# Performance work log

Hardware: AMD Instinct MI355X
Metric: run time of the kernel (lower is better)

Reference implementation:

```python
import jax, jax.numpy as jnp
import numpy as np

N_IMG, N_CAP, N_RGN, MAX_W, EMBED = 32, 32, 36, 50, 1024
LAMBDA_SOFTMAX = 9.0
NORM_EPS = 1e-12  # F.normalize default eps


def setup_inputs() -> dict:
    key = jax.random.key(0)
    ks = jax.random.split(key, 13)
    rgn = jax.random.normal(ks[0], (N_IMG, N_RGN, EMBED), jnp.float32)
    img = jax.random.normal(ks[1], (N_IMG, EMBED), jnp.float32)
    wrd = jax.random.normal(ks[2], (N_CAP, MAX_W, EMBED), jnp.float32)
    stc = jax.random.normal(ks[3], (N_CAP, EMBED), jnp.float32)
    # ragged caption lengths in [1, MAX_W]
    stc_lens = jax.random.randint(ks[4], (N_CAP,), 1, MAX_W + 1, dtype=jnp.int32)
    s = 1.0 / np.sqrt(EMBED)
    w_scale = jax.random.normal(ks[5], (EMBED, EMBED), jnp.float32) * s
    b_scale = jnp.zeros((EMBED,), jnp.float32)
    w_shift = jax.random.normal(ks[6], (EMBED, EMBED), jnp.float32) * s
    b_shift = jnp.zeros((EMBED,), jnp.float32)
    w1 = jax.random.normal(ks[7], (EMBED, EMBED), jnp.float32) * s
    b1 = jnp.zeros((EMBED,), jnp.float32)
    w2 = jax.random.normal(ks[8], (EMBED, EMBED), jnp.float32) * s
    b2 = jnp.zeros((EMBED,), jnp.float32)
    return dict(rgn=rgn, img=img, wrd=wrd, stc=stc, stc_lens=stc_lens,
                w_scale=w_scale, b_scale=b_scale, w_shift=w_shift, b_shift=b_shift,
                w1=w1, b1=b1, w2=w2, b2=b2)


def reference(rgn, img, wrd, stc, stc_lens, w_scale, b_scale, w_shift, b_shift, w1, b1, w2, b2):
    # rgn: (I, Q, D) regions; wrd: (C, L, D) ragged words; stc_lens: (C,)
    C, L, D = wrd.shape
    valid = jnp.arange(L)[None, :] < stc_lens[:, None]          # (C, L)
    # scores[c,i,l,q] = wrd[c,l] . rgn[i,q]  (bmm(context, queryT))
    s = jnp.einsum('cld,iqd->cilq', wrd, rgn)                   # (C, I, L, Q)
    s = jnp.where(s >= 0, s, 0.1 * s)                           # LeakyReLU(0.1)
    # L2-normalize over the query (region) axis, per (c,i,l)
    s = s / jnp.maximum(jnp.sqrt(jnp.sum(s * s, axis=3, keepdims=True)), NORM_EPS)
    # temperature softmax over valid words (ragged mask)
    logits = jnp.where(valid[:, None, :, None], s * LAMBDA_SOFTMAX, -jnp.inf)
    attn = jax.nn.softmax(logits, axis=2)                       # (C, I, L, Q)
    # weightedContext[c,i,q,d] = sum_l attn * wrd
    wei = jnp.einsum('cilq,cld->ciqd', attn, wrd)               # (C, I, Q, D)
    # FiLM-style refine
    scaling = jnp.tanh(jnp.einsum('ciqd,ed->ciqe', wei, w_scale) + b_scale)
    shifting = jnp.einsum('ciqd,ed->ciqe', wei, w_shift) + b_shift
    x = rgn[None] * scaling + shifting                          # (C, I, Q, D)
    h = jax.nn.relu(jnp.einsum('ciqd,ed->ciqe', x, w1) + b1)
    modu = jnp.einsum('ciqd,ed->ciqe', h, w2) + b2
    ref = modu + rgn[None]
    # torch cats per-caption results along dim=1 -> (I, C, Q, D)
    return jnp.transpose(ref, (1, 0, 2, 3))
```

## Files before the change

kernel.cpp:

```cpp
#include <hip/hip_runtime.h>
#include <math.h>

#define NC 32
#define NI 32
#define NL 50
#define NQ 36
#define ND 1024
#define LAMBDA 9.0f

#define BM 128
#define BN 128

typedef __attribute__((ext_vector_type(8))) short bf16x8;
typedef __attribute__((ext_vector_type(4))) float floatx4;

static __device__ __forceinline__ unsigned short f2b(float f) {
    unsigned int u = __float_as_uint(f);
    unsigned int r = (u + 0x7fffu + ((u >> 16) & 1u)) >> 16;
    return (unsigned short)r;
}
static __device__ __forceinline__ float bf2f(unsigned short u) {
    return __uint_as_float(((unsigned int)u) << 16);
}

static __device__ __forceinline__ float ftanh(float x) {
    float ax = fabsf(x);
    float e = __expf(ax + ax);
    return copysignf(1.f - 2.f / (e + 1.f), x);
}

static __device__ __forceinline__ void gload16(const unsigned short* g, unsigned short* l) {
    __builtin_amdgcn_global_load_lds(
        (const __attribute__((address_space(1))) unsigned int*)g,
        (__attribute__((address_space(3))) unsigned int*)l, 16, 0, 0);
}

struct CvtJob { const float* src; unsigned short* dst; int n2; int valid2; };
struct CvtJobs { CvtJob j[4]; };

__global__ __launch_bounds__(256) void k_cvt(CvtJobs jobs) {
    CvtJob jb = jobs.j[blockIdx.y];
    unsigned int* d32 = (unsigned int*)jb.dst;
    int stride = gridDim.x * 256;
    for (int i = blockIdx.x * 256 + threadIdx.x; i < jb.n2; i += stride) {
        unsigned int pk = 0;
        if (i < jb.valid2) {
            float2 v = ((const float2*)jb.src)[i];
            pk = (unsigned int)f2b(v.x) | ((unsigned int)f2b(v.y) << 16);
        }
        d32[i] = pk;
    }
}

struct HlJob { const float* src; unsigned short* hi; unsigned short* lo; int n2; };
struct HlJobs { HlJob j[2]; };

__global__ __launch_bounds__(256) void k_cvt_hilo(HlJobs jobs) {
    HlJob jb = jobs.j[blockIdx.y];
    unsigned int* h32 = (unsigned int*)jb.hi;
    unsigned int* l32 = (unsigned int*)jb.lo;
    int stride = gridDim.x * 256;
    for (int i = blockIdx.x * 256 + threadIdx.x; i < jb.n2; i += stride) {
        float2 v = ((const float2*)jb.src)[i];
        unsigned short h0 = f2b(v.x), h1 = f2b(v.y);
        unsigned short l0 = f2b(v.x - bf2f(h0)), l1 = f2b(v.y - bf2f(h1));
        h32[i] = (unsigned int)h0 | ((unsigned int)h1 << 16);
        l32[i] = (unsigned int)l0 | ((unsigned int)l1 << 16);
    }
}

#define SST 37

__global__ __launch_bounds__(256) void k_attn(
    const unsigned short* __restrict__ whi, const unsigned short* __restrict__ wlo,
    const unsigned short* __restrict__ rhi, const unsigned short* __restrict__ rlo,
    const int* __restrict__ lens, unsigned short* __restrict__ attn)
{
    int bx = blockIdx.x;
    int c = bx / NI, i = bx % NI;
    __shared__ __align__(16) unsigned short Wh[64 * 32], Wl[64 * 32];
    __shared__ __align__(16) unsigned short Rh[48 * 32], Rl[48 * 32];
    __shared__ float S[64 * SST];
    int t = threadIdx.x, lane = t & 63, wid = t >> 6;
    int lrow = lane & 15, quad = lane >> 4;
    int len = lens[c];

    int grow = lane >> 2;
    int ssw = ((lane & 3) ^ ((lane >> 3) & 3)) * 8;
    const unsigned short* garr = (wid == 0) ? whi : (wid == 1) ? wlo : (wid == 2) ? rhi : rlo;
    unsigned short* larr = (wid == 0) ? Wh : (wid == 1) ? Wl : (wid == 2) ? Rh : Rl;
    int ngroups = (wid < 2) ? 4 : 3;
    size_t gbase = (wid < 2) ? (size_t)(c * NL) * ND : (size_t)(i * NQ) * ND;

    floatx4 acc[3] = {};
    int fsw = (quad ^ ((lrow >> 1) & 3)) * 8;

    for (int kt = 0; kt < ND; kt += 32) {
        for (int j = 0; j < ngroups; ++j) {
            int row = j * 16 + grow;
            gload16(garr + gbase + (size_t)row * ND + kt + ssw, larr + j * 512 + lane * 8);
        }
        __syncthreads();
        bf16x8 ah = *(const bf16x8*)&Wh[(wid * 16 + lrow) * 32 + fsw];
        bf16x8 al = *(const bf16x8*)&Wl[(wid * 16 + lrow) * 32 + fsw];
#pragma unroll
        for (int nt = 0; nt < 3; ++nt) {
            bf16x8 bh = *(const bf16x8*)&Rh[(nt * 16 + lrow) * 32 + fsw];
            bf16x8 bl = *(const bf16x8*)&Rl[(nt * 16 + lrow) * 32 + fsw];
            acc[nt] = __builtin_amdgcn_mfma_f32_16x16x32_bf16(ah, bh, acc[nt], 0, 0, 0);
            acc[nt] = __builtin_amdgcn_mfma_f32_16x16x32_bf16(ah, bl, acc[nt], 0, 0, 0);
            acc[nt] = __builtin_amdgcn_mfma_f32_16x16x32_bf16(al, bh, acc[nt], 0, 0, 0);
        }
        __syncthreads();
    }
#pragma unroll
    for (int nt = 0; nt < 3; ++nt) {
        int q = nt * 16 + lrow;
        if (q < NQ) {
#pragma unroll
            for (int r = 0; r < 4; ++r) {
                int l = wid * 16 + quad * 4 + r;
                S[l * SST + q] = acc[nt][r];
            }
        }
    }
    __syncthreads();
    if (t < 200) {
        int l = t >> 2, part = t & 3;
        float lv[9];
        float ss = 0.f;
#pragma unroll
        for (int jj = 0; jj < 9; ++jj) {
            int q = part * 9 + jj;
            float v = S[l * SST + q];
            float x = (v >= 0.f) ? v : 0.1f * v;
            lv[jj] = x;
            ss += x * x;
        }
        ss += __shfl_xor(ss, 1);
        ss += __shfl_xor(ss, 2);
        float inv = LAMBDA / fmaxf(sqrtf(ss), 1e-12f);
#pragma unroll
        for (int jj = 0; jj < 9; ++jj) S[l * SST + part * 9 + jj] = lv[jj] * inv;
    }
    __syncthreads();
    if (t < 144) {
        int q = t >> 2, part = t & 3;
        int ls = part * 13;
        int le = ls + 13 < len ? ls + 13 : len;
        float m = -1e30f;
        for (int l = ls; l < le; ++l) m = fmaxf(m, S[l * SST + q]);
        m = fmaxf(m, __shfl_xor(m, 1));
        m = fmaxf(m, __shfl_xor(m, 2));
        float sum = 0.f;
        for (int l = ls; l < le; ++l) sum += __expf(S[l * SST + q] - m);
        sum += __shfl_xor(sum, 1);
        sum += __shfl_xor(sum, 2);
        float inv = 1.f / sum;
        unsigned int* o = (unsigned int*)attn + ((size_t)(c * NI + i) * NQ + q) * 32;
        int jb = part * 8;
#pragma unroll
        for (int jj = 0; jj < 8; ++jj) {
            int j = jb + jj;
            int l0 = 2 * j, l1 = 2 * j + 1;
            unsigned short a0 = (l0 < len) ? f2b(__expf(S[l0 * SST + q] - m) * inv) : (unsigned short)0;
            unsigned short a1 = (l1 < len) ? f2b(__expf(S[l1 * SST + q] - m) * inv) : (unsigned short)0;
            o[j] = (unsigned int)a0 | ((unsigned int)a1 << 16);
        }
    }
}

__global__ __launch_bounds__(256, 2) void k_pgemm(
    const unsigned short* __restrict__ A, const unsigned short* __restrict__ B1,
    const unsigned short* __restrict__ B2, unsigned short* __restrict__ P1,
    unsigned short* __restrict__ P2)
{
    const int K = ND;
    const int BK = 32;
    int bn = blockIdx.x, bm = blockIdx.y;
    const unsigned short* B = blockIdx.z ? B2 : B1;
    unsigned short* P = blockIdx.z ? P2 : P1;
    int m0 = bm * BM, n0 = bn * BN;

    __shared__ __align__(16) unsigned short At[BM * 32];
    __shared__ __align__(16) unsigned short Bt[BN * 32];

    int t = threadIdx.x, lane = t & 63, wid = t >> 6;
    int wx = wid & 1, wy = wid >> 1;
    int lrow = lane & 15, quad = lane >> 4;
    floatx4 acc[4][4] = {};

    int srow = t >> 2, pos = t & 3;
    int ssw = (pos ^ ((srow >> 1) & 3)) * 8;
    const unsigned short* Aptr = A + (size_t)(m0 + srow) * K + ssw;
    const unsigned short* Bptr = B + (size_t)(n0 + srow) * K + ssw;
    unsigned short* Al  = &At[srow * BK + pos * 8];
    unsigned short* Al2 = &At[(srow + 64) * BK + pos * 8];
    unsigned short* Bl  = &Bt[srow * BK + pos * 8];
    unsigned short* Bl2 = &Bt[(srow + 64) * BK + pos * 8];
    int fsw = (quad ^ ((lrow >> 1) & 3)) * 8;

    for (int kt = 0; kt < K; kt += BK) {
        gload16(Aptr + kt, Al);
        gload16(Aptr + (size_t)64 * K + kt, Al2);
        gload16(Bptr + kt, Bl);
        gload16(Bptr + (size_t)64 * K + kt, Bl2);
        __syncthreads();
        bf16x8 af[4], bfr[4];
#pragma unroll
        for (int im = 0; im < 4; ++im)
            af[im] = *(const bf16x8*)&At[(wy * 64 + im * 16 + lrow) * BK + fsw];
#pragma unroll
        for (int in = 0; in < 4; ++in)
            bfr[in] = *(const bf16x8*)&Bt[(wx * 64 + in * 16 + lrow) * BK + fsw];
#pragma unroll
        for (int im = 0; im < 4; ++im)
#pragma unroll
            for (int in = 0; in < 4; ++in)
                acc[im][in] = __builtin_amdgcn_mfma_f32_16x16x32_bf16(
                    af[im], bfr[in], acc[im][in], 0, 0, 0);
        __syncthreads();
    }
#pragma unroll
    for (int im = 0; im < 4; ++im)
#pragma unroll
        for (int in = 0; in < 4; ++in) {
            int n = n0 + wx * 64 + in * 16 + lrow;
#pragma unroll
            for (int r = 0; r < 4; ++r) {
                int m = m0 + wy * 64 + im * 16 + quad * 4 + r;
                int c = m / NL, l = m - c * NL;
                if (c < NC) P[((size_t)(c * ND + n)) * 64 + l] = f2b(acc[im][in][r]);
            }
        }
}

__global__ __launch_bounds__(256, 2) void k_attn_gemm(
    const unsigned short* __restrict__ attn, const unsigned short* __restrict__ Psc,
    const unsigned short* __restrict__ Psh, const float* __restrict__ bsc,
    const float* __restrict__ bsh, const float* __restrict__ rgnf,
    unsigned short* __restrict__ xbuf)
{
    int bn = blockIdx.x, bm = blockIdx.y, c = blockIdx.z;
    __shared__ __align__(16) unsigned short smem3[3 * 128 * 64];
    unsigned short* At  = smem3;
    unsigned short* B1t = smem3 + 8192;
    unsigned short* B2t = smem3 + 16384;
    unsigned short* Ct  = smem3;
    int t = threadIdx.x, lane = t & 63, wid = t >> 6;
    int wx = wid & 1, wy = wid >> 1;
    int lrow = lane & 15, quad = lane >> 4;
    int grow = lane >> 3, pos = lane & 7;

    const unsigned short* Ab  = attn + (size_t)(c * 1152 + bm * 128) * 64;
    const unsigned short* B1b = Psc + (size_t)(c * ND + bn * 128) * 64;
    const unsigned short* B2b = Psh + (size_t)(c * ND + bn * 128) * 64;
    for (int g = wid; g < 16; g += 4) {
        int row = g * 8 + grow;
        int ssw = (pos ^ (row & 7)) * 8;
        gload16(Ab + (size_t)row * 64 + ssw, &At[g * 512 + lane * 8]);
        gload16(B1b + (size_t)row * 64 + ssw, &B1t[g * 512 + lane * 8]);
        gload16(B2b + (size_t)row * 64 + ssw, &B2t[g * 512 + lane * 8]);
    }
    __syncthreads();

    floatx4 acc[4][4] = {}, acc2[4][4] = {};
#pragma unroll
    for (int kk = 0; kk < 2; ++kk) {
        int sw = ((kk * 4 + quad) ^ (lrow & 7)) * 8;
        bf16x8 af[4], b1f[4], b2f[4];
#pragma unroll
        for (int im = 0; im < 4; ++im)
            af[im] = *(const bf16x8*)&At[(wy * 64 + im * 16 + lrow) * 64 + sw];
#pragma unroll
        for (int in = 0; in < 4; ++in) {
            b1f[in] = *(const bf16x8*)&B1t[(wx * 64 + in * 16 + lrow) * 64 + sw];
            b2f[in] = *(const bf16x8*)&B2t[(wx * 64 + in * 16 + lrow) * 64 + sw];
        }
#pragma unroll
        for (int im = 0; im < 4; ++im)
#pragma unroll
            for (int in = 0; in < 4; ++in) {
                acc[im][in] = __builtin_amdgcn_mfma_f32_16x16x32_bf16(
                    af[im], b1f[in], acc[im][in], 0, 0, 0);
                acc2[im][in] = __builtin_amdgcn_mfma_f32_16x16x32_bf16(
                    af[im], b2f[in], acc2[im][in], 0, 0, 0);
            }
    }
    __syncthreads();
#pragma unroll
    for (int im = 0; im < 4; ++im)
#pragma unroll
        for (int in = 0; in < 4; ++in) {
            int n = bn * 128 + wx * 64 + in * 16 + lrow;
            float b1v = bsc[n], b2v = bsh[n];
#pragma unroll
            for (int r = 0; r < 4; ++r) {
                int row = wy * 64 + im * 16 + quad * 4 + r;
                int m = bm * 128 + row;
                int i = m / NQ, q = m - i * NQ;
                float sc = ftanh(acc[im][in][r] + b1v);
                float sh = acc2[im][in][r] + b2v;
                float rg = rgnf[(size_t)(i * NQ + q) * ND + n];
                int colc = (wx * 8 + in * 2 + (lrow >> 3)) ^ (row & 7);
                Ct[row * 128 + colc * 8 + (lrow & 7)] = f2b(rg * sc + sh);
            }
        }
    __syncthreads();
#pragma unroll
    for (int p = 0; p < 8; ++p) {
        int row = p * 16 + (t >> 4), chunk = t & 15;
        int m = bm * 128 + row;
        int i = m / NQ, q = m - i * NQ;
        size_t dr = ((size_t)(i * NC + c) * NQ + q) * ND + bn * 128 + chunk * 8;
        *(bf16x8*)&xbuf[dr] = *(const bf16x8*)&Ct[row * 128 + ((chunk ^ (row & 7)) * 8)];
    }
}

template <int MODE, int MINW>
__global__ __launch_bounds__(256, MINW) void k_gemm(
    const unsigned short* __restrict__ A, const unsigned short* __restrict__ B1,
    const float* __restrict__ bias1, const float* __restrict__ rgnf,
    void* __restrict__ outp)
{
    const int K = ND;
    int lin = blockIdx.x;
    int xcd = lin & 7;
    int kb = lin >> 3;
    int bm = xcd * 36 + (kb >> 3);
    int bn = kb & 7;
    int m0 = bm * BM, n0 = bn * BN;

    __shared__ __align__(16) unsigned short smem[2 * 128 * 64];
    unsigned short* At = smem;
    unsigned short* Bt = smem + 8192;
    unsigned short* Ct = smem;

    int t = threadIdx.x;
    int lane = t & 63, wid = t >> 6;
    int wx = wid & 1, wy = wid >> 1;
    int lrow = lane & 15, quad = lane >> 4;

    floatx4 acc[4][4] = {};

    int srow = t >> 3, pos = t & 7;
    int ssw = (pos ^ (srow & 7)) * 8;
    const unsigned short* Aptr  = A  + (size_t)(m0 + srow) * K + ssw;
    const unsigned short* B1ptr = B1 + (size_t)(n0 + srow) * K + ssw;
    unsigned short* ldA = At + t * 8;
    unsigned short* ldB = Bt + t * 8;

    for (int kt = 0; kt < K; kt += 64) {
#pragma unroll
        for (int p = 0; p < 4; ++p) {
            gload16(Aptr + (size_t)(p * 32) * K + kt, ldA + p * 2048);
            gload16(B1ptr + (size_t)(p * 32) * K + kt, ldB + p * 2048);
        }
        __syncthreads();
#pragma unroll
        for (int kh = 0; kh < 2; ++kh) {
            int sw = ((kh * 4 + quad) ^ (lrow & 7)) * 8;
            bf16x8 af[4], bfr[4];
#pragma unroll
            for (int im = 0; im < 4; ++im)
                af[im] = *(const bf16x8*)&At[(wy * 64 + im * 16 + lrow) * 64 + sw];
#pragma unroll
            for (int in = 0; in < 4; ++in)
                bfr[in] = *(const bf16x8*)&Bt[(wx * 64 + in * 16 + lrow) * 64 + sw];
#pragma unroll
            for (int im = 0; im < 4; ++im)
#pragma unroll
                for (int in = 0; in < 4; ++in)
                    acc[im][in] = __builtin_amdgcn_mfma_f32_16x16x32_bf16(
                        af[im], bfr[in], acc[im][in], 0, 0, 0);
        }
        __syncthreads();
    }

    if constexpr (MODE == 1) {
#pragma unroll
        for (int im = 0; im < 4; ++im)
#pragma unroll
            for (int in = 0; in < 4; ++in) {
                int n = n0 + wx * 64 + in * 16 + lrow;
                float b1v = bias1[n];
#pragma unroll
                for (int r = 0; r < 4; ++r) {
                    int row = wy * 64 + im * 16 + quad * 4 + r;
                    float h = acc[im][in][r] + b1v;
                    h = h > 0.f ? h : 0.f;
                    int colc = (wx * 8 + in * 2 + (lrow >> 3)) ^ (row & 7);
                    Ct[row * 128 + colc * 8 + (lrow & 7)] = f2b(h);
                }
            }
        __syncthreads();
        unsigned short* ob = (unsigned short*)outp + (size_t)m0 * ND + n0;
#pragma unroll
        for (int p = 0; p < 8; ++p) {
            int row = p * 16 + (t >> 4), chunk = t & 15;
            *(bf16x8*)&ob[(size_t)row * ND + chunk * 8] =
                *(const bf16x8*)&Ct[row * 128 + ((chunk ^ (row & 7)) * 8)];
        }
    } else {
#pragma unroll
        for (int im = 0; im < 4; ++im)
#pragma unroll
            for (int in = 0; in < 4; ++in) {
                int n = n0 + wx * 64 + in * 16 + lrow;
                float b1v = bias1[n];
#pragma unroll
                for (int r = 0; r < 4; ++r) {
                    int m = m0 + wy * 64 + im * 16 + quad * 4 + r;
                    int i = m / (NC * NQ);
                    int q = m % NQ;
                    float rg = rgnf[(size_t)(i * NQ + q) * ND + n];
                    ((float*)outp)[(size_t)m * ND + n] = acc[im][in][r] + b1v + rg;
                }
            }
    }
}

extern "C" void kernel_launch(void* const* d_in, const int* in_sizes, int n_in,
                              void* d_out, int out_size, void* d_ws, size_t ws_size,
                              hipStream_t stream) {
    const float* rgn     = (const float*)d_in[0];
    const float* wrd     = (const float*)d_in[2];
    const int*   lens    = (const int*)d_in[4];
    const float* w_scale = (const float*)d_in[5];
    const float* b_scale = (const float*)d_in[6];
    const float* w_shift = (const float*)d_in[7];
    const float* b_shift = (const float*)d_in[8];
    const float* w1      = (const float*)d_in[9];
    const float* b1      = (const float*)d_in[10];
    const float* w2      = (const float*)d_in[11];
    const float* b2      = (const float*)d_in[12];
    float* outf = (float*)d_out;

    char* ws = (char*)d_ws;
    unsigned short* wsc_bf = (unsigned short*)(ws + 0);
    unsigned short* wsh_bf = (unsigned short*)(ws + 2097152);
    unsigned short* w1_bf  = (unsigned short*)(ws + 4194304);
    unsigned short* w2_bf  = (unsigned short*)(ws + 6291456);
    unsigned short* attn   = (unsigned short*)(ws + 11796480);
    unsigned short* P_sct  = (unsigned short*)(ws + 16515072);
    unsigned short* P_sht  = (unsigned short*)(ws + 20709376);
    unsigned short* wrd_hi = (unsigned short*)(ws + 24903680);
    unsigned short* wrd_lo = (unsigned short*)(ws + 28209152);
    unsigned short* rgn_hi = (unsigned short*)(ws + 31514624);
    unsigned short* rgn_lo = (unsigned short*)(ws + 33898496);
    unsigned short* hbuf   = (unsigned short*)(ws + 8388608);
    unsigned short* xbuf   = (unsigned short*)d_out;

    CvtJobs jobs;
    jobs.j[0] = { w_scale, wsc_bf, ND * ND / 2, ND * ND / 2 };
    jobs.j[1] = { w_shift, wsh_bf, ND * ND / 2, ND * ND / 2 };
    jobs.j[2] = { w1,      w1_bf,  ND * ND / 2, ND * ND / 2 };
    jobs.j[3] = { w2,      w2_bf,  ND * ND / 2, ND * ND / 2 };
    k_cvt<<<dim3(128, 4), 256, 0, stream>>>(jobs);

    HlJobs hjobs;
    hjobs.j[0] = { wrd, wrd_hi, wrd_lo, NC * NL * ND / 2 };
    hjobs.j[1] = { rgn, rgn_hi, rgn_lo, NI * NQ * ND / 2 };
    k_cvt_hilo<<<dim3(128, 2), 256, 0, stream>>>(hjobs);

    k_attn<<<NC * NI, 256, 0, stream>>>(wrd_hi, wrd_lo, rgn_hi, rgn_lo, lens, attn);

    k_pgemm<<<dim3(8, 13, 2), 256, 0, stream>>>(wrd_hi, wsc_bf, wsh_bf, P_sct, P_sht);

    k_attn_gemm<<<dim3(8, 9, 32), 256, 0, stream>>>(attn, P_sct, P_sht,
                                                    b_scale, b_shift, rgn, xbuf);

    k_gemm<1, 2><<<2304, 256, 0, stream>>>(xbuf, w1_bf, b1, rgn, hbuf);
    k_gemm<2, 2><<<2304, 256, 0, stream>>>(hbuf, w2_bf, b2, rgn, outf);
}
```

Before: 446.3 us.

## Batch word-region scores into one large split-bf16 GEMM before softmax

Replaces the per-(caption,image) score kernel, which recomputed a small 50x36 tile and reloaded operands per block, with a single tiled 128x128 GEMM over all words and regions writing fp32 scores to a workspace buffer. A separate softmax kernel then reads each caption-image slice back from global memory. This improves operand reuse but adds a global round trip of the score matrix, an extra launch, and a grid of only 117 blocks.

```diff
diff --git a/kernel.cpp b/kernel.cpp
--- a/kernel.cpp
+++ b/kernel.cpp
@@ -69,60 +69,95 @@
     }
 }
 
+__global__ __launch_bounds__(256, 2) void k_sgemm(
+    const unsigned short* __restrict__ Ah_, const unsigned short* __restrict__ Al_,
+    const unsigned short* __restrict__ Bh_, const unsigned short* __restrict__ Bl_,
+    float* __restrict__ Sb)
+{
+    const int K = ND;
+    const int BK = 32;
+    int bn = blockIdx.x, bm = blockIdx.y;
+    int m0 = bm * 128, n0 = bn * 128;
+
+    __shared__ __align__(16) unsigned short Aht[128 * 32], Alt[128 * 32];
+    __shared__ __align__(16) unsigned short Bht[128 * 32], Blt[128 * 32];
+
+    int t = threadIdx.x, lane = t & 63, wid = t >> 6;
+    int wx = wid & 1, wy = wid >> 1;
+    int lrow = lane & 15, quad = lane >> 4;
+    floatx4 acc[4][4] = {};
+
+    int srow = t >> 2, pos = t & 3;
+    int ssw = (pos ^ ((srow >> 1) & 3)) * 8;
+    const unsigned short* Ahp = Ah_ + (size_t)(m0 + srow) * K + ssw;
+    const unsigned short* Alp = Al_ + (size_t)(m0 + srow) * K + ssw;
+    const unsigned short* Bhp = Bh_ + (size_t)(n0 + srow) * K + ssw;
+    const unsigned short* Blp = Bl_ + (size_t)(n0 + srow) * K + ssw;
+    int dst0 = srow * BK + pos * 8;
+    int fsw = (quad ^ ((lrow >> 1) & 3)) * 8;
+
+    for (int kt = 0; kt < K; kt += BK) {
+        gload16(Ahp + kt, &Aht[dst0]);
+        gload16(Ahp + (size_t)64 * K + kt, &Aht[dst0 + 2048]);
+        gload16(Alp + kt, &Alt[dst0]);
+        gload16(Alp + (size_t)64 * K + kt, &Alt[dst0 + 2048]);
+        gload16(Bhp + kt, &Bht[dst0]);
+        gload16(Bhp + (size_t)64 * K + kt, &Bht[dst0 + 2048]);
+        gload16(Blp + kt, &Blt[dst0]);
+        gload16(Blp + (size_t)64 * K + kt, &Blt[dst0 + 2048]);
+        __syncthreads();
+        bf16x8 ah[4], al[4], bh[4], bl[4];
+#pragma unroll
+        for (int im = 0; im < 4; ++im) {
+            ah[im] = *(const bf16x8*)&Aht[(wy * 64 + im * 16 + lrow) * BK + fsw];
+            al[im] = *(const bf16x8*)&Alt[(wy * 64 + im * 16 + lrow) * BK + fsw];
+        }
+#pragma unroll
+        for (int in = 0; in < 4; ++in) {
+            bh[in] = *(const bf16x8*)&Bht[(wx * 64 + in * 16 + lrow) * BK + fsw];
+            bl[in] = *(const bf16x8*)&Blt[(wx * 64 + in * 16 + lrow) * BK + fsw];
+        }
+#pragma unroll
+        for (int im = 0; im < 4; ++im)
+#pragma unroll
+            for (int in = 0; in < 4; ++in) {
+                acc[im][in] = __builtin_amdgcn_mfma_f32_16x16x32_bf16(
+                    ah[im], bh[in], acc[im][in], 0, 0, 0);
+                acc[im][in] = __builtin_amdgcn_mfma_f32_16x16x32_bf16(
+                    ah[im], bl[in], acc[im][in], 0, 0, 0);
+                acc[im][in] = __builtin_amdgcn_mfma_f32_16x16x32_bf16(
+                    al[im], bh[in], acc[im][in], 0, 0, 0);
+            }
+        __syncthreads();
+    }
+#pragma unroll
+    for (int im = 0; im < 4; ++im)
+#pragma unroll
+        for (int in = 0; in < 4; ++in) {
+            int n = n0 + wx * 64 + in * 16 + lrow;
+#pragma unroll
+            for (int r = 0; r < 4; ++r) {
+                int m = m0 + wy * 64 + im * 16 + quad * 4 + r;
+                if (m < NC * NL) Sb[(size_t)m * (NI * NQ) + n] = acc[im][in][r];
+            }
+        }
+}
+
 #define SST 37
 
-__global__ __launch_bounds__(256) void k_attn(
-    const unsigned short* __restrict__ whi, const unsigned short* __restrict__ wlo,
-    const unsigned short* __restrict__ rhi, const unsigned short* __restrict__ rlo,
-    const int* __restrict__ lens, unsigned short* __restrict__ attn)
+__global__ __launch_bounds__(256) void k_softmax(
+    const float* __restrict__ Sb, const int* __restrict__ lens,
+    unsigned short* __restrict__ attn)
 {
     int bx = blockIdx.x;
     int c = bx / NI, i = bx % NI;
-    __shared__ __align__(16) unsigned short Wh[64 * 32], Wl[64 * 32];
-    __shared__ __align__(16) unsigned short Rh[48 * 32], Rl[48 * 32];
-    __shared__ float S[64 * SST];
-    int t = threadIdx.x, lane = t & 63, wid = t >> 6;
-    int lrow = lane & 15, quad = lane >> 4;
+    __shared__ float S[NL * SST];
+    int t = threadIdx.x;
     int len = lens[c];
 
-    int grow = lane >> 2;
-    int ssw = ((lane & 3) ^ ((lane >> 3) & 3)) * 8;
-    const unsigned short* garr = (wid == 0) ? whi : (wid == 1) ? wlo : (wid == 2) ? rhi : rlo;
-    unsigned short* larr = (wid == 0) ? Wh : (wid == 1) ? Wl : (wid == 2) ? Rh : Rl;
-    int ngroups = (wid < 2) ? 4 : 3;
-    size_t gbase = (wid < 2) ? (size_t)(c * NL) * ND : (size_t)(i * NQ) * ND;
-
-    floatx4 acc[3] = {};
-    int fsw = (quad ^ ((lrow >> 1) & 3)) * 8;
-
-    for (int kt = 0; kt < ND; kt += 32) {
-        for (int j = 0; j < ngroups; ++j) {
-            int row = j * 16 + grow;
-            gload16(garr + gbase + (size_t)row * ND + kt + ssw, larr + j * 512 + lane * 8);
-        }
-        __syncthreads();
-        bf16x8 ah = *(const bf16x8*)&Wh[(wid * 16 + lrow) * 32 + fsw];
-        bf16x8 al = *(const bf16x8*)&Wl[(wid * 16 + lrow) * 32 + fsw];
-#pragma unroll
-        for (int nt = 0; nt < 3; ++nt) {
-            bf16x8 bh = *(const bf16x8*)&Rh[(nt * 16 + lrow) * 32 + fsw];
-            bf16x8 bl = *(const bf16x8*)&Rl[(nt * 16 + lrow) * 32 + fsw];
-            acc[nt] = __builtin_amdgcn_mfma_f32_16x16x32_bf16(ah, bh, acc[nt], 0, 0, 0);
-            acc[nt] = __builtin_amdgcn_mfma_f32_16x16x32_bf16(ah, bl, acc[nt], 0, 0, 0);
-            acc[nt] = __builtin_amdgcn_mfma_f32_16x16x32_bf16(al, bh, acc[nt], 0, 0, 0);
-        }
-        __syncthreads();
-    }
-#pragma unroll
-    for (int nt = 0; nt < 3; ++nt) {
-        int q = nt * 16 + lrow;
-        if (q < NQ) {
-#pragma unroll
-            for (int r = 0; r < 4; ++r) {
-                int l = wid * 16 + quad * 4 + r;
-                S[l * SST + q] = acc[nt][r];
-            }
-        }
+    for (int idx = t; idx < NL * NQ; idx += 256) {
+        int l = idx / NQ, q = idx - l * NQ;
+        S[l * SST + q] = Sb[(size_t)(c * NL + l) * (NI * NQ) + i * NQ + q];
     }
     __syncthreads();
     if (t < 200) {
@@ -448,6 +483,7 @@
     unsigned short* wrd_lo = (unsigned short*)(ws + 28209152);
     unsigned short* rgn_hi = (unsigned short*)(ws + 31514624);
     unsigned short* rgn_lo = (unsigned short*)(ws + 33898496);
+    float*          S_big  = (float*)(ws + 36282368);
     unsigned short* hbuf   = (unsigned short*)(ws + 8388608);
     unsigned short* xbuf   = (unsigned short*)d_out;
 
@@ -463,7 +499,8 @@
     hjobs.j[1] = { rgn, rgn_hi, rgn_lo, NI * NQ * ND / 2 };
     k_cvt_hilo<<<dim3(128, 2), 256, 0, stream>>>(hjobs);
 
-    k_attn<<<NC * NI, 256, 0, stream>>>(wrd_hi, wrd_lo, rgn_hi, rgn_lo, lens, attn);
+    k_sgemm<<<dim3(9, 13), 256, 0, stream>>>(wrd_hi, wrd_lo, rgn_hi, rgn_lo, S_big);
+    k_softmax<<<NC * NI, 256, 0, stream>>>(S_big, lens, attn);
 
     k_pgemm<<<dim3(8, 13, 2), 256, 0, stream>>>(wrd_hi, wsc_bf, wsh_bf, P_sct, P_sht);
 
```

Result: no change. 454.4 us (+1.8%).
